# Optimization experiments

Hardware: AMD Instinct MI355X
Metric: run time of the kernel (lower is better)

Reference implementation:

```python
import jax, jax.numpy as jnp
import numpy as np

NUM_EXPERTS = 64
TOP_K = 2
NOISE_STD = 1.0
LOAD_BALANCE_WEIGHT = 0.01
NOISE_KEY = jax.random.fold_in(jax.random.key(0), 12345)


def setup_inputs() -> dict:
    key = jax.random.key(0)
    k1, k2, k3 = jax.random.split(key, 3)
    B, S, D = 4, 4096, 1024
    x = jax.random.normal(k1, (B, S, D), dtype=jnp.float32)
    W_gate = jax.random.normal(k2, (NUM_EXPERTS, D), dtype=jnp.float32) * (1.0 / np.sqrt(D))
    W_noise = jax.random.normal(k3, (NUM_EXPERTS, D), dtype=jnp.float32) * (1.0 / np.sqrt(D))
    return {"x": x, "W_gate": W_gate, "W_noise": W_noise}


def reference(x, W_gate, W_noise):
    # x: [B,S,D], W_gate/W_noise: [E,D] (torch Linear weight layout)
    clean_logits = jnp.einsum("bsd,ed->bse", x, W_gate)           # [B,S,E]
    noise_scale = jax.nn.softplus(jnp.einsum("bsd,ed->bse", x, W_noise))
    noise = jax.random.normal(NOISE_KEY, clean_logits.shape, clean_logits.dtype)
    logits = clean_logits + noise * noise_scale * NOISE_STD

    probs = jax.nn.softmax(logits, axis=-1)                        # [B,S,E]
    routing_weights, expert_indices = jax.lax.top_k(probs, TOP_K)  # [B,S,K]
    routing_weights = routing_weights / jnp.sum(routing_weights, axis=-1, keepdims=True)

    # Load-balance loss on clean logits
    B, S, E = clean_logits.shape
    num_tokens = B * S
    expert_mask = jax.nn.one_hot(expert_indices, E, dtype=jnp.float32).sum(axis=2)  # [B,S,E]
    tokens_per_expert = expert_mask.sum(axis=(0, 1))               # [E]
    fraction_tokens = tokens_per_expert / num_tokens
    router_probs = jax.nn.softmax(clean_logits, axis=-1)
    mean_router_prob = router_probs.mean(axis=(0, 1))              # [E]
    load_balance_loss = LOAD_BALANCE_WEIGHT * E * jnp.sum(fraction_tokens * mean_router_prob)

    noise_scale_mean = noise_scale.mean()
    return (routing_weights, expert_indices, load_balance_loss, router_probs, noise_scale_mean)
```

## Files before the change

### kernel.cpp

```cpp
#include <hip/hip_runtime.h>
#include <stdint.h>

#define TOKENS 16384
#define DDIM   1024
#define NEXP   64
#define NCOL   128
#define TB     32
#define NBLK   (TOKENS / TB)
#define NCH    (DDIM / 32)
#define NTILE  8
#define CPP    8

typedef __attribute__((ext_vector_type(8))) short bf16x8;
typedef __attribute__((ext_vector_type(4))) float f32x4;

__device__ ushort g_wf[3][NTILE][NCH][64][8];
__device__ float g_ps[NEXP];
__device__ float g_cnt[NEXP];
__device__ float g_spa[1];

__device__ inline ushort bf16rne(float f) {
  uint32_t u = __float_as_uint(f);
  return (ushort)((u + 0x7fffu + ((u >> 16) & 1u)) >> 16);
}
__device__ inline float bf16tof(ushort h) {
  return __uint_as_float(((uint32_t)h) << 16);
}
__device__ inline void split3(float v, ushort& h, ushort& m, ushort& l) {
  h = bf16rne(v);
  float r1 = v - bf16tof(h);
  m = bf16rne(r1);
  float r2 = r1 - bf16tof(m);
  l = bf16rne(r2);
}

struct U2 { uint32_t a, b; };

__host__ __device__ constexpr U2 tf2x32(uint32_t k0, uint32_t k1,
                                        uint32_t x0, uint32_t x1) {
  uint32_t ks[3] = {k0, k1, k0 ^ k1 ^ 0x1BD11BDAu};
  const uint32_t rot[2][4] = {{13u, 15u, 26u, 6u}, {17u, 29u, 16u, 24u}};
  x0 += ks[0]; x1 += ks[1];
  for (int d = 0; d < 5; ++d) {
    for (int j = 0; j < 4; ++j) {
      uint32_t r = rot[d & 1][j];
      x0 += x1;
      x1 = (x1 << r) | (x1 >> (32u - r));
      x1 ^= x0;
    }
    x0 += ks[(d + 1) % 3];
    x1 += ks[(d + 2) % 3] + (uint32_t)(d + 1);
  }
  return U2{x0, x1};
}

__device__ inline uint32_t noise_bits(uint32_t i) {
  constexpr U2 NK = tf2x32(0u, 0u, 0u, 12345u);
  U2 o = tf2x32(NK.a, NK.b, 0u, i);
  return o.a ^ o.b;
}

__device__ inline float xla_erfinv(float x) {
  float w = -log1pf(-x * x);
  float p;
  if (w < 5.0f) {
    w = w - 2.5f;
    p = 2.81022636e-08f;
    p = 3.43273939e-07f + p * w;
    p = -3.5233877e-06f + p * w;
    p = -4.39150654e-06f + p * w;
    p = 0.00021858087f + p * w;
    p = -0.00125372503f + p * w;
    p = -0.00417768164f + p * w;
    p = 0.246640727f + p * w;
    p = 1.50140941f + p * w;
  } else {
    w = sqrtf(w) - 3.0f;
    p = -0.000200214257f;
    p = 0.000100950558f + p * w;
    p = 0.00134934322f + p * w;
    p = -0.00367342844f + p * w;
    p = 0.00573950773f + p * w;
    p = -0.0076224613f + p * w;
    p = 0.00943887047f + p * w;
    p = 1.00167406f + p * w;
    p = 2.83297682f + p * w;
  }
  return p * x;
}

__device__ inline float noise_normal(uint32_t i) {
  uint32_t bits = noise_bits(i);
  float f = __uint_as_float((bits >> 9) | 0x3f800000u) - 1.0f;
  float u = f * 2.0f + (-0.99999994f);
  u = fmaxf(u, -0.99999994f);
  return 1.41421356237f * xla_erfinv(u);
}

__device__ inline float softplus_ref(float x) {
  return fmaxf(x, 0.0f) + log1pf(expf(-fabsf(x)));
}

__device__ inline float wave_max64(float v) {
  #pragma unroll
  for (int off = 32; off; off >>= 1) v = fmaxf(v, __shfl_xor(v, off, 64));
  return v;
}
__device__ inline float wave_sum64(float v) {
  #pragma unroll
  for (int off = 32; off; off >>= 1) v += __shfl_xor(v, off, 64);
  return v;
}
__device__ inline void wave_argmax64(float v, int idx, float& mv, int& mi) {
  float bv = v; int bi = idx;
  #pragma unroll
  for (int off = 32; off; off >>= 1) {
    float ov = __shfl_xor(bv, off, 64);
    int   oi = __shfl_xor(bi, off, 64);
    if (ov > bv || (ov == bv && oi < bi)) { bv = ov; bi = oi; }
  }
  mv = bv; mi = bi;
}

__global__ __launch_bounds__(64)
void wsplit_kernel(const float* __restrict__ wg, const float* __restrict__ wn) {
  const int ct   = blockIdx.x >> 5;
  const int kc   = blockIdx.x & 31;
  const int lane = threadIdx.x;
  const int col  = ct * 16 + (lane & 15);
  const int koff = kc * 32 + (lane >> 4) * 8;
  const float* src = (col < NEXP) ? (wg + (size_t)col * DDIM)
                                  : (wn + (size_t)(col - NEXP) * DDIM);
  const float4 v0 = *(const float4*)&src[koff];
  const float4 v1 = *(const float4*)&src[koff + 4];
  const float av[8] = {v0.x, v0.y, v0.z, v0.w, v1.x, v1.y, v1.z, v1.w};
  union BF8 { bf16x8 v; ushort u[8]; };
  BF8 H, M, L;
  #pragma unroll
  for (int j = 0; j < 8; ++j) {
    ushort h, m, l;
    split3(av[j], h, m, l);
    H.u[j] = h; M.u[j] = m; L.u[j] = l;
  }
  *(bf16x8*)&g_wf[0][ct][kc][lane][0] = H.v;
  *(bf16x8*)&g_wf[1][ct][kc][lane][0] = M.v;
  *(bf16x8*)&g_wf[2][ct][kc][lane][0] = L.v;

  if (blockIdx.x == 0) {
    g_ps[lane] = 0.0f; g_cnt[lane] = 0.0f;
    if (lane == 0) g_spa[0] = 0.0f;
  }
}

#define PHASE_BARRIER()                                      \
  asm volatile("s_waitcnt lgkmcnt(0)" ::: "memory");         \
  __builtin_amdgcn_s_barrier();                              \
  asm volatile("" ::: "memory");

__global__ __launch_bounds__(1024, 8)
void NoisyTopKRouter_57621281243491_kernel(
    const float* __restrict__ x, float* __restrict__ out) {
  __shared__ ushort ldsA[3][2][CPP][64][8];

  const int tid  = threadIdx.x;
  const int w    = tid >> 6;
  const int lane = tid & 63;
  const int tg   = w & 1;
  const int ct   = w >> 1;
  const int tok0 = blockIdx.x * TB;

  char* LA = (char*)&ldsA[0][0][0][0][0];

  const int srow = tid >> 5;
  const int skq  = tid & 31;
  const int stg  = srow >> 4;
  const int sfr  = srow & 15;
  const int sc   = skq >> 2;
  const int ss   = skq & 3;
  const int so   = (sc * 1024 + ss * 256 + sfr * 16) ^ ((skq & 15) << 4);
  const float* sx = x + (size_t)(tok0 + srow) * DDIM + skq * 8;

  const int fr_row = lane & 15;
  const int fr_s   = lane >> 4;
  const ushort* wf = &g_wf[0][0][0][0][0];
  const int b0 = ct * 16384 + lane * 8;
  #define PS 131072
  const int abase = tg * 8192;

  f32x4 acc = {0.f, 0.f, 0.f, 0.f};

  float4 xa0, xa1, xb0, xb1;

  #define SPLIT_PHASE(X0, X1)                                             \
    {                                                                     \
      union BF8 { bf16x8 v; ushort u[8]; };                               \
      BF8 H, M, L;                                                        \
      const float av_[8] = {X0.x, X0.y, X0.z, X0.w, X1.x, X1.y, X1.z, X1.w}; \
      _Pragma("unroll")                                                   \
      for (int j = 0; j < 8; ++j) {                                       \
        ushort h_, m_, l_;                                                \
        split3(av_[j], h_, m_, l_);                                       \
        H.u[j] = h_; M.u[j] = m_; L.u[j] = l_;                            \
      }                                                                   \
      *(bf16x8*)(LA + stg * 8192 + so)         = H.v;                     \
      *(bf16x8*)(LA + 16384 + stg * 8192 + so) = M.v;                     \
      *(bf16x8*)(LA + 32768 + stg * 8192 + so) = L.v;                     \
    }

  #define MFMA_PHASE(ph)                                                  \
    __builtin_amdgcn_s_setprio(1);                                        \
    _Pragma("unroll")                                                     \
    for (int c = 0; c < CPP; ++c) {                                       \
      int ro = c * 1024 + lane * 16;                                      \
      ro ^= ((ro >> 8) & 15) << 4;                                        \
      const bf16x8 Ah = *(const bf16x8*)(LA + abase + ro);                \
      const bf16x8 Am = *(const bf16x8*)(LA + 16384 + abase + ro);        \
      const bf16x8 Al = *(const bf16x8*)(LA + 32768 + abase + ro);        \
      const int co = ((ph) * CPP + c) * 512;                              \
      const bf16x8 Bh = *(const bf16x8*)&wf[b0 + co];                     \
      const bf16x8 Bm = *(const bf16x8*)&wf[b0 + PS + co];                \
      const bf16x8 Bl = *(const bf16x8*)&wf[b0 + 2 * PS + co];            \
      acc = __builtin_amdgcn_mfma_f32_16x16x32_bf16(Ah, Bh, acc, 0, 0, 0); \
      acc = __builtin_amdgcn_mfma_f32_16x16x32_bf16(Ah, Bm, acc, 0, 0, 0); \
      acc = __builtin_amdgcn_mfma_f32_16x16x32_bf16(Am, Bh, acc, 0, 0, 0); \
      acc = __builtin_amdgcn_mfma_f32_16x16x32_bf16(Ah, Bl, acc, 0, 0, 0); \
      acc = __builtin_amdgcn_mfma_f32_16x16x32_bf16(Al, Bh, acc, 0, 0, 0); \
      acc = __builtin_amdgcn_mfma_f32_16x16x32_bf16(Am, Bm, acc, 0, 0, 0); \
    }                                                                     \
    __builtin_amdgcn_s_setprio(0);

  #define DO_PHASE(ph, C0, C1, N0, N1, PRE)                               \
    SPLIT_PHASE(C0, C1);                                                  \
    if (PRE) {                                                            \
      N0 = *(const float4*)&sx[(ph + 1) * 256];                           \
      N1 = *(const float4*)&sx[(ph + 1) * 256 + 4];                       \
    }                                                                     \
    PHASE_BARRIER();                                                      \
    MFMA_PHASE(ph);                                                       \
    PHASE_BARRIER();

  xa0 = *(const float4*)&sx[0];
  xa1 = *(const float4*)&sx[4];

  DO_PHASE(0, xa0, xa1, xb0, xb1, 1);
  DO_PHASE(1, xb0, xb1, xa0, xa1, 1);
  DO_PHASE(2, xa0, xa1, xb0, xb1, 1);
  DO_PHASE(3, xb0, xb1, xa0, xa1, 0);

  #undef DO_PHASE
  #undef SPLIT_PHASE
  #undef MFMA_PHASE
  #undef PS

  float (*lds_logits)[NCOL + 4] = (float (*)[NCOL + 4])LA;
  float (*lps)[NEXP] = (float (*)[NEXP])(LA + 16896);
  float (*lcb)[NEXP] = (float (*)[NEXP])(LA + 20992);
  float* lspw        = (float*)(LA + 25088);

  #pragma unroll
  for (int r = 0; r < 4; ++r)
    lds_logits[tg * 16 + 4 * fr_s + r][ct * 16 + fr_row] = acc[r];
  __syncthreads();

  float* out_rw  = out;
  float* out_idx = out + 2 * TOKENS;
  float* out_rp  = out + 4 * TOKENS + 1;

  float ps_acc = 0.0f, sp_acc = 0.0f, c_acc = 0.0f;

  for (int it = 0; it < 2; ++it) {
    const int tl = w * 2 + it;
    const int t  = tok0 + tl;
    const float cl = lds_logits[tl][lane];
    const float nl = lds_logits[tl][NEXP + lane];

    const float m  = wave_max64(cl);
    const float v  = expf(cl - m);
    const float Z  = wave_sum64(v);
    const float rp = v / Z;
    out_rp[(size_t)t * NEXP + lane] = rp;
    ps_acc += rp;

    const float ns  = softplus_ref(nl);
    sp_acc += ns;
    const float noi = noise_normal((uint32_t)(t * NEXP + lane));
    const float lgn = __fadd_rn(cl, __fmul_rn(noi, ns));

    const float m2 = wave_max64(lgn);
    const float v2 = expf(lgn - m2);
    const float Z2 = wave_sum64(v2);
    const float p  = v2 / Z2;

    float p1; int i1;
    wave_argmax64(p, lane, p1, i1);
    const float pm = (lane == i1) ? -3.402823466e38f : p;
    float p2; int i2;
    wave_argmax64(pm, lane, p2, i2);

    c_acc += (float)((lane == i1) + (lane == i2));

    if (lane == 0) {
      const float s = p1 + p2;
      out_rw[t * 2 + 0]  = p1 / s;
      out_rw[t * 2 + 1]  = p2 / s;
      out_idx[t * 2 + 0] = (float)i1;
      out_idx[t * 2 + 1] = (float)i2;
    }
  }

  lps[w][lane] = ps_acc;
  lcb[w][lane] = c_acc;
  const float spw = wave_sum64(sp_acc);
  if (lane == 0) lspw[w] = spw;
  __syncthreads();
  if (tid < NEXP) {
    float a = 0.0f, b = 0.0f;
    #pragma unroll
    for (int j = 0; j < 16; ++j) { a += lps[j][tid]; b += lcb[j][tid]; }
    atomicAdd(&g_ps[tid],  a);
    atomicAdd(&g_cnt[tid], b);
  }
  if (tid == 0) {
    float s = 0.0f;
    #pragma unroll
    for (int j = 0; j < 16; ++j) s += lspw[j];
    atomicAdd(&g_spa[0], s);
  }
}

__global__ void finalize_kernel(float* __restrict__ out) {
  const int lane = threadIdx.x;
  float term = (g_cnt[lane] / (float)TOKENS) * (g_ps[lane] / (float)TOKENS);
  #pragma unroll
  for (int off = 32; off; off >>= 1) term += __shfl_xor(term, off, 64);
  if (lane == 0) {
    out[4 * TOKENS] = 0.64f * term;
    out[4 * TOKENS + 1 + TOKENS * NEXP] = g_spa[0] / (float)(TOKENS * NEXP);
  }
}

extern "C" void kernel_launch(void* const* d_in, const int* in_sizes, int n_in,
                              void* d_out, int out_size, void* d_ws, size_t ws_size,
                              hipStream_t stream) {
  const float* x  = (const float*)d_in[0];
  const float* wg = (const float*)d_in[1];
  const float* wn = (const float*)d_in[2];
  float* out = (float*)d_out;

  (void)d_ws; (void)ws_size; (void)in_sizes; (void)n_in; (void)out_size;

  wsplit_kernel<<<NTILE * NCH, 64, 0, stream>>>(wg, wn);
  NoisyTopKRouter_57621281243491_kernel<<<NBLK, 1024, 0, stream>>>(x, out);
  finalize_kernel<<<1, 64, 0, stream>>>(out);
}
```

Measured before the change: 144.2 us.

## Double tokens per block so each wave reuses B fragments across two token tiles

Raises the token tile per block from 32 to 64 and halves chunks per phase, running eight phases instead of four. Each wave now keeps two accumulators and issues MFMAs for two 16-token tiles against the same loaded weight fragments, halving global weight-fragment reads per token. The trade is more registers, a larger LDS footprint, fewer blocks (launch bounds lowered to 4), and twice as many barrier phases.

```diff
diff --git a/kernel.cpp b/kernel.cpp
--- a/kernel.cpp
+++ b/kernel.cpp
@@ -5,11 +5,11 @@
 #define DDIM   1024
 #define NEXP   64
 #define NCOL   128
-#define TB     32
+#define TB     64
 #define NBLK   (TOKENS / TB)
 #define NCH    (DDIM / 32)
 #define NTILE  8
-#define CPP    8
+#define CPP    4
 
 typedef __attribute__((ext_vector_type(8))) short bf16x8;
 typedef __attribute__((ext_vector_type(4))) float f32x4;
@@ -157,22 +157,22 @@
   __builtin_amdgcn_s_barrier();                              \
   asm volatile("" ::: "memory");
 
-__global__ __launch_bounds__(1024, 8)
+__global__ __launch_bounds__(1024, 4)
 void NoisyTopKRouter_57621281243491_kernel(
     const float* __restrict__ x, float* __restrict__ out) {
-  __shared__ ushort ldsA[3][2][CPP][64][8];
+  __shared__ ushort ldsA[3][4][CPP][64][8];
 
   const int tid  = threadIdx.x;
   const int w    = tid >> 6;
   const int lane = tid & 63;
-  const int tg   = w & 1;
   const int ct   = w >> 1;
+  const int tgp  = w & 1;
   const int tok0 = blockIdx.x * TB;
 
   char* LA = (char*)&ldsA[0][0][0][0][0];
 
-  const int srow = tid >> 5;
-  const int skq  = tid & 31;
+  const int srow = tid >> 4;
+  const int skq  = tid & 15;
   const int stg  = srow >> 4;
   const int sfr  = srow & 15;
   const int sc   = skq >> 2;
@@ -185,9 +185,11 @@
   const ushort* wf = &g_wf[0][0][0][0][0];
   const int b0 = ct * 16384 + lane * 8;
   #define PS 131072
-  const int abase = tg * 8192;
-
-  f32x4 acc = {0.f, 0.f, 0.f, 0.f};
+  const int abA = (tgp * 2) * 4096;
+  const int abB = abA + 4096;
+
+  f32x4 accA = {0.f, 0.f, 0.f, 0.f};
+  f32x4 accB = {0.f, 0.f, 0.f, 0.f};
 
   float4 xa0, xa1, xb0, xb1;
 
@@ -202,9 +204,9 @@
         split3(av_[j], h_, m_, l_);                                       \
         H.u[j] = h_; M.u[j] = m_; L.u[j] = l_;                            \
       }                                                                   \
-      *(bf16x8*)(LA + stg * 8192 + so)         = H.v;                     \
-      *(bf16x8*)(LA + 16384 + stg * 8192 + so) = M.v;                     \
-      *(bf16x8*)(LA + 32768 + stg * 8192 + so) = L.v;                     \
+      *(bf16x8*)(LA + stg * 4096 + so)         = H.v;                     \
+      *(bf16x8*)(LA + 16384 + stg * 4096 + so) = M.v;                     \
+      *(bf16x8*)(LA + 32768 + stg * 4096 + so) = L.v;                     \
     }
 
   #define MFMA_PHASE(ph)                                                  \
@@ -213,27 +215,36 @@
     for (int c = 0; c < CPP; ++c) {                                       \
       int ro = c * 1024 + lane * 16;                                      \
       ro ^= ((ro >> 8) & 15) << 4;                                        \
-      const bf16x8 Ah = *(const bf16x8*)(LA + abase + ro);                \
-      const bf16x8 Am = *(const bf16x8*)(LA + 16384 + abase + ro);        \
-      const bf16x8 Al = *(const bf16x8*)(LA + 32768 + abase + ro);        \
+      const bf16x8 AhA = *(const bf16x8*)(LA + abA + ro);                 \
+      const bf16x8 AmA = *(const bf16x8*)(LA + 16384 + abA + ro);         \
+      const bf16x8 AlA = *(const bf16x8*)(LA + 32768 + abA + ro);         \
+      const bf16x8 AhB = *(const bf16x8*)(LA + abB + ro);                 \
+      const bf16x8 AmB = *(const bf16x8*)(LA + 16384 + abB + ro);         \
+      const bf16x8 AlB = *(const bf16x8*)(LA + 32768 + abB + ro);         \
       const int co = ((ph) * CPP + c) * 512;                              \
       const bf16x8 Bh = *(const bf16x8*)&wf[b0 + co];                     \
       const bf16x8 Bm = *(const bf16x8*)&wf[b0 + PS + co];                \
       const bf16x8 Bl = *(const bf16x8*)&wf[b0 + 2 * PS + co];            \
-      acc = __builtin_amdgcn_mfma_f32_16x16x32_bf16(Ah, Bh, acc, 0, 0, 0); \
-      acc = __builtin_amdgcn_mfma_f32_16x16x32_bf16(Ah, Bm, acc, 0, 0, 0); \
-      acc = __builtin_amdgcn_mfma_f32_16x16x32_bf16(Am, Bh, acc, 0, 0, 0); \
-      acc = __builtin_amdgcn_mfma_f32_16x16x32_bf16(Ah, Bl, acc, 0, 0, 0); \
-      acc = __builtin_amdgcn_mfma_f32_16x16x32_bf16(Al, Bh, acc, 0, 0, 0); \
-      acc = __builtin_amdgcn_mfma_f32_16x16x32_bf16(Am, Bm, acc, 0, 0, 0); \
+      accA = __builtin_amdgcn_mfma_f32_16x16x32_bf16(AhA, Bh, accA, 0, 0, 0); \
+      accA = __builtin_amdgcn_mfma_f32_16x16x32_bf16(AhA, Bm, accA, 0, 0, 0); \
+      accA = __builtin_amdgcn_mfma_f32_16x16x32_bf16(AmA, Bh, accA, 0, 0, 0); \
+      accA = __builtin_amdgcn_mfma_f32_16x16x32_bf16(AhA, Bl, accA, 0, 0, 0); \
+      accA = __builtin_amdgcn_mfma_f32_16x16x32_bf16(AlA, Bh, accA, 0, 0, 0); \
+      accA = __builtin_amdgcn_mfma_f32_16x16x32_bf16(AmA, Bm, accA, 0, 0, 0); \
+      accB = __builtin_amdgcn_mfma_f32_16x16x32_bf16(AhB, Bh, accB, 0, 0, 0); \
+      accB = __builtin_amdgcn_mfma_f32_16x16x32_bf16(AhB, Bm, accB, 0, 0, 0); \
+      accB = __builtin_amdgcn_mfma_f32_16x16x32_bf16(AmB, Bh, accB, 0, 0, 0); \
+      accB = __builtin_amdgcn_mfma_f32_16x16x32_bf16(AhB, Bl, accB, 0, 0, 0); \
+      accB = __builtin_amdgcn_mfma_f32_16x16x32_bf16(AlB, Bh, accB, 0, 0, 0); \
+      accB = __builtin_amdgcn_mfma_f32_16x16x32_bf16(AmB, Bm, accB, 0, 0, 0); \
     }                                                                     \
     __builtin_amdgcn_s_setprio(0);
 
   #define DO_PHASE(ph, C0, C1, N0, N1, PRE)                               \
     SPLIT_PHASE(C0, C1);                                                  \
     if (PRE) {                                                            \
-      N0 = *(const float4*)&sx[(ph + 1) * 256];                           \
-      N1 = *(const float4*)&sx[(ph + 1) * 256 + 4];                       \
+      N0 = *(const float4*)&sx[(ph + 1) * 128];                           \
+      N1 = *(const float4*)&sx[(ph + 1) * 128 + 4];                       \
     }                                                                     \
     PHASE_BARRIER();                                                      \
     MFMA_PHASE(ph);                                                       \
@@ -245,7 +256,11 @@
   DO_PHASE(0, xa0, xa1, xb0, xb1, 1);
   DO_PHASE(1, xb0, xb1, xa0, xa1, 1);
   DO_PHASE(2, xa0, xa1, xb0, xb1, 1);
-  DO_PHASE(3, xb0, xb1, xa0, xa1, 0);
+  DO_PHASE(3, xb0, xb1, xa0, xa1, 1);
+  DO_PHASE(4, xa0, xa1, xb0, xb1, 1);
+  DO_PHASE(5, xb0, xb1, xa0, xa1, 1);
+  DO_PHASE(6, xa0, xa1, xb0, xb1, 1);
+  DO_PHASE(7, xb0, xb1, xa0, xa1, 0);
 
   #undef DO_PHASE
   #undef SPLIT_PHASE
@@ -253,13 +268,15 @@
   #undef PS
 
   float (*lds_logits)[NCOL + 4] = (float (*)[NCOL + 4])LA;
-  float (*lps)[NEXP] = (float (*)[NEXP])(LA + 16896);
-  float (*lcb)[NEXP] = (float (*)[NEXP])(LA + 20992);
-  float* lspw        = (float*)(LA + 25088);
-
-  #pragma unroll
-  for (int r = 0; r < 4; ++r)
-    lds_logits[tg * 16 + 4 * fr_s + r][ct * 16 + fr_row] = acc[r];
+  float (*lps)[NEXP] = (float (*)[NEXP])(LA + 33792);
+  float (*lcb)[NEXP] = (float (*)[NEXP])(LA + 37888);
+  float* lspw        = (float*)(LA + 41984);
+
+  #pragma unroll
+  for (int r = 0; r < 4; ++r) {
+    lds_logits[(tgp * 2) * 16 + 4 * fr_s + r][ct * 16 + fr_row]     = accA[r];
+    lds_logits[(tgp * 2 + 1) * 16 + 4 * fr_s + r][ct * 16 + fr_row] = accB[r];
+  }
   __syncthreads();
 
   float* out_rw  = out;
@@ -268,8 +285,8 @@
 
   float ps_acc = 0.0f, sp_acc = 0.0f, c_acc = 0.0f;
 
-  for (int it = 0; it < 2; ++it) {
-    const int tl = w * 2 + it;
+  for (int it = 0; it < 4; ++it) {
+    const int tl = w * 4 + it;
     const int t  = tok0 + tl;
     const float cl = lds_logits[tl][lane];
     const float nl = lds_logits[tl][NEXP + lane];
```

Result: faster. 138.3 us (-4.1%).
